# Performance work log

Hardware: AMD Instinct MI355X
Metric: run time of the kernel (lower is better)

The kernel has to match this reference:

```python
import jax, jax.numpy as jnp
import numpy as np

N_LAYERS = 3
N_HEADS = 16
EMB = 1024
HEAD_DIM = EMB // N_HEADS
BLOCK = 1024
VOCAB = 32000
LN_EPS = 1e-5


def _layernorm(x, g, b):
    mu = jnp.mean(x, axis=-1, keepdims=True)
    var = jnp.mean((x - mu) ** 2, axis=-1, keepdims=True)
    return (x - mu) * jax.lax.rsqrt(var + LN_EPS) * g + b


def setup_inputs() -> dict:
    key = jax.random.key(0)
    ks = jax.random.split(key, 20)
    s = 0.02
    inp = {
        "input_ids": jax.random.randint(ks[0], (4, 1024), 0, VOCAB),
        "targets": jax.random.randint(ks[1], (4, 1024), 0, VOCAB),
        "tok_emb": jax.random.normal(ks[2], (VOCAB, EMB), jnp.float32) * s,
        "pos_emb": jax.random.normal(ks[3], (BLOCK, EMB), jnp.float32) * s,
        # per-layer stacked params [L, ...]
        "wq": jax.random.normal(ks[4], (N_LAYERS, N_HEADS, EMB, HEAD_DIM), jnp.float32) * s,
        "wk": jax.random.normal(ks[5], (N_LAYERS, N_HEADS, EMB, HEAD_DIM), jnp.float32) * s,
        "wv": jax.random.normal(ks[6], (N_LAYERS, N_HEADS, EMB, HEAD_DIM), jnp.float32) * s,
        "wo": jax.random.normal(ks[7], (N_LAYERS, EMB, EMB), jnp.float32) * s,
        "bo": jnp.zeros((N_LAYERS, EMB), jnp.float32),
        "ln1_g": jnp.ones((N_LAYERS, EMB), jnp.float32),
        "ln1_b": jnp.zeros((N_LAYERS, EMB), jnp.float32),
        "w1": jax.random.normal(ks[8], (N_LAYERS, EMB, 4 * EMB), jnp.float32) * s,
        "b1": jnp.zeros((N_LAYERS, 4 * EMB), jnp.float32),
        "w2": jax.random.normal(ks[9], (N_LAYERS, 4 * EMB, EMB), jnp.float32) * s,
        "b2": jnp.zeros((N_LAYERS, EMB), jnp.float32),
        "lnf_g": jnp.ones((EMB,), jnp.float32),
        "lnf_b": jnp.zeros((EMB,), jnp.float32),
        "lm_w": jax.random.normal(ks[10], (EMB, VOCAB), jnp.float32) * s,
        "lm_b": jnp.zeros((VOCAB,), jnp.float32),
    }
    return inp


def _forward(input_ids, targets, tok_emb, pos_emb, wq, wk, wv, wo, bo,
             ln1_g, ln1_b, w1, b1, w2, b2, lnf_g, lnf_b, lm_w, lm_b):
    B, T = input_ids.shape
    x = tok_emb[input_ids] + pos_emb[:T]  # [B,T,E]
    scale = 1.0 / np.sqrt(EMB)  # NOTE: original scales by 1/sqrt(C)=1/sqrt(emb_dim)
    causal = jnp.tril(jnp.ones((T, T), bool))
    for l in range(N_LAYERS):
        h = _layernorm(x, ln1_g[l], ln1_b[l])
        q = jnp.einsum('bte,hed->bhtd', h, wq[l])
        k = jnp.einsum('bte,hed->bhtd', h, wk[l])
        v = jnp.einsum('bte,hed->bhtd', h, wv[l])
        wei = jnp.einsum('bhtd,bhsd->bhts', q, k) * scale
        wei = jnp.where(causal, wei, -jnp.inf)
        wei = jax.nn.softmax(wei, axis=-1)  # dropout = identity (eval)
        o = jnp.einsum('bhts,bhsd->bhtd', wei, v)
        o = o.transpose(0, 2, 1, 3).reshape(B, T, EMB)  # concat heads
        x = x + jnp.einsum('bte,ef->btf', o, wo[l]) + bo[l]
        # NOTE: original Block applies ln1 (not ln2) before the FFN too
        h2 = _layernorm(x, ln1_g[l], ln1_b[l])
        ff = jax.nn.relu(jnp.einsum('bte,ef->btf', h2, w1[l]) + b1[l])
        x = x + jnp.einsum('btf,fe->bte', ff, w2[l]) + b2[l]
    x = _layernorm(x, lnf_g, lnf_b)
    logits = jnp.einsum('bte,ev->btv', x, lm_w) + lm_b
    logits = logits.reshape(B * T, VOCAB)
    tgt = targets.reshape(B * T)
    logp = jax.nn.log_softmax(logits, axis=-1)
    loss = -jnp.mean(jnp.take_along_axis(logp, tgt[:, None], axis=-1))
    return logits, loss


def reference(input_ids, targets, tok_emb, pos_emb, wq, wk, wv, wo, bo,
              ln1_g, ln1_b, w1, b1, w2, b2, lnf_g, lnf_b, lm_w, lm_b):
    return _forward(input_ids, targets, tok_emb, pos_emb, wq, wk, wv, wo, bo,
                    ln1_g, ln1_b, w1, b1, w2, b2, lnf_g, lnf_b, lm_w, lm_b)
```

## Files before the change

### kernel.cpp

```cpp
#include <hip/hip_runtime.h>
#include <hip/hip_bf16.h>
#include <stdint.h>

#define EMB    1024
#define NH     16
#define HD     64
#define SEQ    1024
#define NBATCH 4
#define NTOK   4096
#define VOCAB  32000
#define NL     3
#define FFD    4096
#define LN_EPS 1e-5f

typedef __attribute__((ext_vector_type(8))) __bf16 bf16x8;
typedef __attribute__((ext_vector_type(4))) float  f32x4;

__device__ inline unsigned short f2b(float f) {
  __hip_bfloat16 h = __float2bfloat16(f);
  return *reinterpret_cast<unsigned short*>(&h);
}
__device__ inline float b2f(unsigned short u) {
  unsigned x = ((unsigned)u) << 16;
  return __uint_as_float(x);
}

__global__ __launch_bounds__(256) void gemm_bt(
    const unsigned short* __restrict__ A,
    const unsigned short* __restrict__ Bt,
    float* __restrict__ Cf,
    unsigned short* __restrict__ Cb,
    const float* __restrict__ resid,
    const float* __restrict__ bias,
    int M, int N, int K,
    int lda, int ldb, int ldc,
    int nb2, long sa1, long sa2, long sb1, long sb2, long sc1, long sc2,
    float scale, int flags)
{
  __shared__ __align__(16) unsigned short As[128 * 40];
  __shared__ __align__(16) unsigned short Bs[128 * 40];

  int z  = blockIdx.z;
  int i1 = z / nb2, i2 = z - i1 * nb2;
  long aoff = (long)i1 * sa1 + (long)i2 * sa2;
  long boff = (long)i1 * sb1 + (long)i2 * sb2;
  long coff = (long)i1 * sc1 + (long)i2 * sc2;

  int n0 = blockIdx.x * 128;
  int m0 = blockIdx.y * 128;

  int t    = threadIdx.x;
  int wave = t >> 6, lane = t & 63;
  int wm   = wave >> 1, wn = wave & 1;
  int quad = lane >> 4, l16 = lane & 15;

  f32x4 acc[4][4];
#pragma unroll
  for (int i = 0; i < 4; ++i)
#pragma unroll
    for (int j = 0; j < 4; ++j)
      acc[i][j] = (f32x4){0.f, 0.f, 0.f, 0.f};

  int r_st = t >> 2;
  int s_st = t & 3;

  for (int kt = 0; kt < K; kt += 32) {
    __syncthreads();
#pragma unroll
    for (int it = 0; it < 2; ++it) {
      int r  = r_st + it * 64;
      int gk = kt + s_st * 8;
      uint4 va = make_uint4(0u, 0u, 0u, 0u);
      int gm = m0 + r;
      if (gm < M) va = *(const uint4*)(A + aoff + (long)gm * lda + gk);
      *(uint4*)&As[r * 40 + s_st * 8] = va;
      uint4 vb = make_uint4(0u, 0u, 0u, 0u);
      int gn = n0 + r;
      if (gn < N) vb = *(const uint4*)(Bt + boff + (long)gn * ldb + gk);
      *(uint4*)&Bs[r * 40 + s_st * 8] = vb;
    }
    __syncthreads();

    bf16x8 af[4], bv[4];
#pragma unroll
    for (int i = 0; i < 4; ++i)
      af[i] = *(const bf16x8*)&As[(wm * 64 + i * 16 + l16) * 40 + quad * 8];
#pragma unroll
    for (int j = 0; j < 4; ++j)
      bv[j] = *(const bf16x8*)&Bs[(wn * 64 + j * 16 + l16) * 40 + quad * 8];
#pragma unroll
    for (int i = 0; i < 4; ++i)
#pragma unroll
      for (int j = 0; j < 4; ++j)
        acc[i][j] = __builtin_amdgcn_mfma_f32_16x16x32_bf16(af[i], bv[j], acc[i][j], 0, 0, 0);
  }

#pragma unroll
  for (int i = 0; i < 4; ++i) {
#pragma unroll
    for (int j = 0; j < 4; ++j) {
#pragma unroll
      for (int r = 0; r < 4; ++r) {
        int m = m0 + wm * 64 + i * 16 + quad * 4 + r;
        int n = n0 + wn * 64 + j * 16 + l16;
        if (m < M && n < N) {
          float v = acc[i][j][r] * scale;
          if ((flags & 2) && n > m) v = -__builtin_inff();
          if (bias)  v += bias[n];
          if (resid) v += resid[coff + (long)m * ldc + n];
          if (flags & 1) v = fmaxf(v, 0.f);
          long off = coff + (long)m * ldc + n;
          if (Cb) Cb[off] = f2b(v);
          else    Cf[off] = v;
        }
      }
    }
  }
}

__global__ void transpose_fb(const float* __restrict__ in, unsigned short* __restrict__ out,
                             int R, int C, int ld_in,
                             int nb2, long is1, long is2, long os1, long os2)
{
  __shared__ float tile[32][33];
  int z = blockIdx.z;
  int i1 = z / nb2, i2 = z - i1 * nb2;
  const float* ip = in + (long)i1 * is1 + (long)i2 * is2;
  unsigned short* op = out + (long)i1 * os1 + (long)i2 * os2;
  int c0 = blockIdx.x * 32, r0 = blockIdx.y * 32;
  int tx = threadIdx.x, ty = threadIdx.y;
#pragma unroll
  for (int i = 0; i < 32; i += 8) {
    int r = r0 + ty + i, c = c0 + tx;
    if (r < R && c < C) tile[ty + i][tx] = ip[(long)r * ld_in + c];
  }
  __syncthreads();
#pragma unroll
  for (int i = 0; i < 32; i += 8) {
    int c = c0 + ty + i, r = r0 + tx;
    if (r < R && c < C) op[(long)c * R + r] = f2b(tile[tx][ty + i]);
  }
}

__global__ void transpose_bb(const unsigned short* __restrict__ in, unsigned short* __restrict__ out,
                             int R, int C, int ld_in,
                             int nb2, long is1, long is2, long os1, long os2)
{
  __shared__ unsigned short tile[32][33];
  int z = blockIdx.z;
  int i1 = z / nb2, i2 = z - i1 * nb2;
  const unsigned short* ip = in + (long)i1 * is1 + (long)i2 * is2;
  unsigned short* op = out + (long)i1 * os1 + (long)i2 * os2;
  int c0 = blockIdx.x * 32, r0 = blockIdx.y * 32;
  int tx = threadIdx.x, ty = threadIdx.y;
#pragma unroll
  for (int i = 0; i < 32; i += 8) {
    int r = r0 + ty + i, c = c0 + tx;
    if (r < R && c < C) tile[ty + i][tx] = ip[(long)r * ld_in + c];
  }
  __syncthreads();
#pragma unroll
  for (int i = 0; i < 32; i += 8) {
    int c = c0 + ty + i, r = r0 + tx;
    if (r < R && c < C) op[(long)c * R + r] = tile[tx][ty + i];
  }
}

__global__ void embed_k(const int* __restrict__ ids, const float* __restrict__ tok,
                        const float* __restrict__ pos, float* __restrict__ x)
{
  int row = blockIdx.x;
  int tp  = row & (SEQ - 1);
  int id  = ids[row];
  const float* tr = tok + (long)id * EMB;
  const float* pr = pos + (long)tp * EMB;
  float* xr = x + (long)row * EMB;
  for (int i = threadIdx.x; i < EMB; i += 256) xr[i] = tr[i] + pr[i];
}

__global__ void ln_k(const float* __restrict__ x, const float* __restrict__ g,
                     const float* __restrict__ b, unsigned short* __restrict__ h)
{
  __shared__ float sm[8];
  int row = blockIdx.x;
  const float* xr = x + (long)row * EMB;
  float v[4]; float s = 0.f, s2 = 0.f;
#pragma unroll
  for (int i = 0; i < 4; ++i) {
    v[i] = xr[threadIdx.x + i * 256];
    s += v[i]; s2 += v[i] * v[i];
  }
  for (int off = 32; off > 0; off >>= 1) {
    s  += __shfl_down(s,  off, 64);
    s2 += __shfl_down(s2, off, 64);
  }
  int wave = threadIdx.x >> 6, lane = threadIdx.x & 63;
  if (lane == 0) { sm[wave * 2] = s; sm[wave * 2 + 1] = s2; }
  __syncthreads();
  s  = sm[0] + sm[2] + sm[4] + sm[6];
  s2 = sm[1] + sm[3] + sm[5] + sm[7];
  float mu  = s * (1.f / EMB);
  float var = s2 * (1.f / EMB) - mu * mu;
  float inv = rsqrtf(var + LN_EPS);
  unsigned short* hr = h + (long)row * EMB;
#pragma unroll
  for (int i = 0; i < 4; ++i) {
    int e = threadIdx.x + i * 256;
    hr[e] = f2b((v[i] - mu) * inv * g[e] + b[e]);
  }
}

__global__ void softmax_k(unsigned short* __restrict__ S)
{
  __shared__ float sm[4];
  long row = blockIdx.x;
  unsigned short* r = S + row * 1024;
  float v[4]; float mx = -__builtin_inff();
#pragma unroll
  for (int i = 0; i < 4; ++i) { v[i] = b2f(r[threadIdx.x + i * 256]); mx = fmaxf(mx, v[i]); }
  for (int off = 32; off > 0; off >>= 1) mx = fmaxf(mx, __shfl_down(mx, off, 64));
  int wave = threadIdx.x >> 6, lane = threadIdx.x & 63;
  if (lane == 0) sm[wave] = mx;
  __syncthreads();
  mx = fmaxf(fmaxf(sm[0], sm[1]), fmaxf(sm[2], sm[3]));
  __syncthreads();
  float e[4]; float s = 0.f;
#pragma unroll
  for (int i = 0; i < 4; ++i) { e[i] = __expf(v[i] - mx); s += e[i]; }
  for (int off = 32; off > 0; off >>= 1) s += __shfl_down(s, off, 64);
  if (lane == 0) sm[wave] = s;
  __syncthreads();
  s = sm[0] + sm[1] + sm[2] + sm[3];
  float inv = 1.f / s;
#pragma unroll
  for (int i = 0; i < 4; ++i) r[threadIdx.x + i * 256] = f2b(e[i] * inv);
}

__global__ void loss_rows_k(const float* __restrict__ logits, const int* __restrict__ tgt,
                            float* __restrict__ rowloss)
{
  __shared__ float smm[4], sms[4];
  int row = blockIdx.x;
  const float* lr = logits + (long)row * VOCAB;
  float m = -__builtin_inff(), s = 0.f;
  for (int i = threadIdx.x; i < VOCAB; i += 256) {
    float x = lr[i];
    float nm = fmaxf(m, x);
    s = s * __expf(m - nm) + __expf(x - nm);
    m = nm;
  }
  for (int off = 32; off > 0; off >>= 1) {
    float om = __shfl_down(m, off, 64);
    float os = __shfl_down(s, off, 64);
    float nm = fmaxf(m, om);
    s = s * __expf(m - nm) + os * __expf(om - nm);
    m = nm;
  }
  int wave = threadIdx.x >> 6, lane = threadIdx.x & 63;
  if (lane == 0) { smm[wave] = m; sms[wave] = s; }
  __syncthreads();
  if (threadIdx.x == 0) {
    float M0 = fmaxf(fmaxf(smm[0], smm[1]), fmaxf(smm[2], smm[3]));
    float S0 = 0.f;
    for (int w = 0; w < 4; ++w) S0 += sms[w] * __expf(smm[w] - M0);
    rowloss[row] = M0 + logf(S0) - lr[tgt[row]];
  }
}

__global__ void loss_reduce_k(const float* __restrict__ rowloss, float* __restrict__ out)
{
  __shared__ float sm[4];
  float s = 0.f;
  for (int i = threadIdx.x; i < NTOK; i += 256) s += rowloss[i];
  for (int off = 32; off > 0; off >>= 1) s += __shfl_down(s, off, 64);
  int wave = threadIdx.x >> 6, lane = threadIdx.x & 63;
  if (lane == 0) sm[wave] = s;
  __syncthreads();
  if (threadIdx.x == 0) out[0] = (sm[0] + sm[1] + sm[2] + sm[3]) * (1.f / NTOK);
}

extern "C" void kernel_launch(void* const* d_in, const int* in_sizes, int n_in,
                              void* d_out, int out_size, void* d_ws, size_t ws_size,
                              hipStream_t stream)
{
  const int*   ids  = (const int*)d_in[0];
  const int*   tgt  = (const int*)d_in[1];
  const float* tok  = (const float*)d_in[2];
  const float* pos  = (const float*)d_in[3];
  const float* wq   = (const float*)d_in[4];
  const float* wk   = (const float*)d_in[5];
  const float* wv   = (const float*)d_in[6];
  const float* wo   = (const float*)d_in[7];
  const float* bo   = (const float*)d_in[8];
  const float* ln1g = (const float*)d_in[9];
  const float* ln1b = (const float*)d_in[10];
  const float* w1   = (const float*)d_in[11];
  const float* b1   = (const float*)d_in[12];
  const float* w2   = (const float*)d_in[13];
  const float* b2   = (const float*)d_in[14];
  const float* lnfg = (const float*)d_in[15];
  const float* lnfb = (const float*)d_in[16];
  const float* lmw  = (const float*)d_in[17];
  const float* lmb  = (const float*)d_in[18];

  float* logits = (float*)d_out;
  float* loss   = logits + (long)NTOK * VOCAB;

  char* p = (char*)d_ws;
  auto alloc = [&](size_t bytes) { char* q = p; p += (bytes + 255) & ~(size_t)255; return q; };
  float*          x    = (float*)alloc((size_t)NTOK * EMB * 4);
  unsigned short* h    = (unsigned short*)alloc((size_t)NTOK * EMB * 2);
  unsigned short* qkv  = (unsigned short*)alloc((size_t)NTOK * 3 * EMB * 2);
  unsigned short* vT   = (unsigned short*)alloc((size_t)NBATCH * NH * HD * SEQ * 2);
  unsigned short* S    = (unsigned short*)alloc((size_t)NBATCH * NH * SEQ * SEQ * 2);
  unsigned short* o    = (unsigned short*)alloc((size_t)NTOK * EMB * 2);
  unsigned short* ff   = (unsigned short*)alloc((size_t)NTOK * FFD * 2);
  unsigned short* Wqkv = (unsigned short*)alloc((size_t)NL * 3 * EMB * EMB * 2);
  unsigned short* Wo   = (unsigned short*)alloc((size_t)NL * EMB * EMB * 2);
  unsigned short* W1   = (unsigned short*)alloc((size_t)NL * EMB * FFD * 2);
  unsigned short* W2   = (unsigned short*)alloc((size_t)NL * EMB * FFD * 2);
  unsigned short* LM   = (unsigned short*)alloc((size_t)VOCAB * EMB * 2);
  float*          rls  = (float*)alloc((size_t)NTOK * 4);

  dim3 tb(32, 8);
  const long LEE = (long)EMB * EMB;

  for (int l = 0; l < NL; ++l) {
    transpose_fb<<<dim3(2, 32, 16), tb, 0, stream>>>(wq + (long)l * NH * EMB * HD,
        Wqkv + (long)l * 3 * LEE,            EMB, HD, HD, 16, 0, (long)EMB * HD, 0, (long)HD * EMB);
    transpose_fb<<<dim3(2, 32, 16), tb, 0, stream>>>(wk + (long)l * NH * EMB * HD,
        Wqkv + (long)l * 3 * LEE + LEE,      EMB, HD, HD, 16, 0, (long)EMB * HD, 0, (long)HD * EMB);
    transpose_fb<<<dim3(2, 32, 16), tb, 0, stream>>>(wv + (long)l * NH * EMB * HD,
        Wqkv + (long)l * 3 * LEE + 2 * LEE,  EMB, HD, HD, 16, 0, (long)EMB * HD, 0, (long)HD * EMB);
    transpose_fb<<<dim3(32, 32, 1), tb, 0, stream>>>(wo + l * LEE, Wo + l * LEE,
        EMB, EMB, EMB, 1, 0, 0, 0, 0);
    transpose_fb<<<dim3(128, 32, 1), tb, 0, stream>>>(w1 + (long)l * EMB * FFD, W1 + (long)l * EMB * FFD,
        EMB, FFD, FFD, 1, 0, 0, 0, 0);
    transpose_fb<<<dim3(32, 128, 1), tb, 0, stream>>>(w2 + (long)l * EMB * FFD, W2 + (long)l * EMB * FFD,
        FFD, EMB, EMB, 1, 0, 0, 0, 0);
  }
  transpose_fb<<<dim3(1000, 32, 1), tb, 0, stream>>>(lmw, LM, EMB, VOCAB, VOCAB, 1, 0, 0, 0, 0);

  embed_k<<<NTOK, 256, 0, stream>>>(ids, tok, pos, x);

  for (int l = 0; l < NL; ++l) {
    const float* g1  = ln1g + l * EMB;
    const float* bb1 = ln1b + l * EMB;

    ln_k<<<NTOK, 256, 0, stream>>>(x, g1, bb1, h);

    gemm_bt<<<dim3(24, 32, 1), 256, 0, stream>>>(h, Wqkv + (long)l * 3 * LEE, nullptr, qkv,
        nullptr, nullptr, NTOK, 3 * EMB, EMB, EMB, EMB, 3 * EMB,
        1, 0, 0, 0, 0, 0, 0, 1.f, 0);

    transpose_bb<<<dim3(2, 32, NBATCH * NH), tb, 0, stream>>>(qkv + 2 * EMB, vT,
        SEQ, HD, 3 * EMB, NH, (long)SEQ * 3 * EMB, (long)HD, (long)NH * HD * SEQ, (long)HD * SEQ);

    gemm_bt<<<dim3(8, 8, NBATCH * NH), 256, 0, stream>>>(qkv, qkv + EMB, nullptr, S,
        nullptr, nullptr, SEQ, SEQ, HD, 3 * EMB, 3 * EMB, SEQ,
        NH, (long)SEQ * 3 * EMB, (long)HD, (long)SEQ * 3 * EMB, (long)HD,
        (long)NH * SEQ * SEQ, (long)SEQ * SEQ, 0.03125f, 2);

    softmax_k<<<NBATCH * NH * SEQ, 256, 0, stream>>>(S);

    gemm_bt<<<dim3(1, 8, NBATCH * NH), 256, 0, stream>>>(S, vT, nullptr, o,
        nullptr, nullptr, SEQ, HD, SEQ, SEQ, SEQ, EMB,
        NH, (long)NH * SEQ * SEQ, (long)SEQ * SEQ, (long)NH * HD * SEQ, (long)HD * SEQ,
        (long)SEQ * EMB, (long)HD, 1.f, 0);

    gemm_bt<<<dim3(8, 32, 1), 256, 0, stream>>>(o, Wo + l * LEE, x, nullptr,
        x, bo + l * EMB, NTOK, EMB, EMB, EMB, EMB, EMB,
        1, 0, 0, 0, 0, 0, 0, 1.f, 0);

    ln_k<<<NTOK, 256, 0, stream>>>(x, g1, bb1, h);

    gemm_bt<<<dim3(32, 32, 1), 256, 0, stream>>>(h, W1 + (long)l * EMB * FFD, nullptr, ff,
        nullptr, b1 + l * FFD, NTOK, FFD, EMB, EMB, EMB, FFD,
        1, 0, 0, 0, 0, 0, 0, 1.f, 1);

    gemm_bt<<<dim3(8, 32, 1), 256, 0, stream>>>(ff, W2 + (long)l * EMB * FFD, x, nullptr,
        x, b2 + l * EMB, NTOK, EMB, FFD, FFD, FFD, EMB,
        1, 0, 0, 0, 0, 0, 0, 1.f, 0);
  }

  ln_k<<<NTOK, 256, 0, stream>>>(x, lnfg, lnfb, h);
  gemm_bt<<<dim3(250, 32, 1), 256, 0, stream>>>(h, LM, logits, nullptr,
      nullptr, lmb, NTOK, VOCAB, EMB, EMB, EMB, VOCAB,
      1, 0, 0, 0, 0, 0, 0, 1.f, 0);

  loss_rows_k<<<NTOK, 256, 0, stream>>>(logits, tgt, rls);
  loss_reduce_k<<<1, 256, 0, stream>>>(rls, loss);
}
```

Measured before the change: 3.565 ms.

## Use direct global-to-LDS loads, XCD-aware tile remap, and skip masked causal tiles

```diff
diff --git a/kernel.cpp b/kernel.cpp
--- a/kernel.cpp
+++ b/kernel.cpp
@@ -23,6 +23,12 @@
 __device__ inline float b2f(unsigned short u) {
   unsigned x = ((unsigned)u) << 16;
   return __uint_as_float(x);
+}
+
+__device__ inline void gload16(const void* g, void* l) {
+  __builtin_amdgcn_global_load_lds(
+      (const __attribute__((address_space(1))) unsigned int*)g,
+      (__attribute__((address_space(3))) unsigned int*)l, 16, 0, 0);
 }
 
 __global__ __launch_bounds__(256) void gemm_bt(
@@ -37,8 +43,8 @@
     int nb2, long sa1, long sa2, long sb1, long sb2, long sc1, long sc2,
     float scale, int flags)
 {
-  __shared__ __align__(16) unsigned short As[128 * 40];
-  __shared__ __align__(16) unsigned short Bs[128 * 40];
+  __shared__ __align__(16) unsigned short As[128 * 32];
+  __shared__ __align__(16) unsigned short Bs[128 * 32];
 
   int z  = blockIdx.z;
   int i1 = z / nb2, i2 = z - i1 * nb2;
@@ -46,14 +52,36 @@
   long boff = (long)i1 * sb1 + (long)i2 * sb2;
   long coff = (long)i1 * sc1 + (long)i2 * sc2;
 
-  int n0 = blockIdx.x * 128;
-  int m0 = blockIdx.y * 128;
+  int flat = blockIdx.y * gridDim.x + blockIdx.x;
+  int nwg  = gridDim.x * gridDim.y;
+  if (gridDim.z == 1 && nwg > 8) {
+    int q = nwg >> 3, rq = nwg & 7;
+    int xcd = flat & 7, idx = flat >> 3;
+    flat = (xcd < rq ? xcd * (q + 1) : rq * (q + 1) + (xcd - rq) * q) + idx;
+  }
+  int n0 = (flat % gridDim.x) * 128;
+  int m0 = (flat / gridDim.x) * 128;
 
   int t    = threadIdx.x;
   int wave = t >> 6, lane = t & 63;
   int wm   = wave >> 1, wn = wave & 1;
   int quad = lane >> 4, l16 = lane & 15;
 
+  if ((flags & 2) && n0 >= m0 + 128) {
+    unsigned short ninf = f2b(-__builtin_inff());
+#pragma unroll
+    for (int i = 0; i < 4; ++i)
+#pragma unroll
+      for (int j = 0; j < 4; ++j)
+#pragma unroll
+        for (int r = 0; r < 4; ++r) {
+          int m = m0 + wm * 64 + i * 16 + quad * 4 + r;
+          int n = n0 + wn * 64 + j * 16 + l16;
+          if (m < M && n < N) Cb[coff + (long)m * ldc + n] = ninf;
+        }
+    return;
+  }
+
   f32x4 acc[4][4];
 #pragma unroll
   for (int i = 0; i < 4; ++i)
@@ -61,33 +89,29 @@
     for (int j = 0; j < 4; ++j)
       acc[i][j] = (f32x4){0.f, 0.f, 0.f, 0.f};
 
-  int r_st = t >> 2;
-  int s_st = t & 3;
+  const unsigned short* Ag = A + aoff;
+  const unsigned short* Bg = Bt + boff;
+  int srow = wave * 16 + (lane >> 2);
+  int kcol = (lane & 3) * 8;
 
   for (int kt = 0; kt < K; kt += 32) {
     __syncthreads();
 #pragma unroll
-    for (int it = 0; it < 2; ++it) {
-      int r  = r_st + it * 64;
-      int gk = kt + s_st * 8;
-      uint4 va = make_uint4(0u, 0u, 0u, 0u);
-      int gm = m0 + r;
-      if (gm < M) va = *(const uint4*)(A + aoff + (long)gm * lda + gk);
-      *(uint4*)&As[r * 40 + s_st * 8] = va;
-      uint4 vb = make_uint4(0u, 0u, 0u, 0u);
-      int gn = n0 + r;
-      if (gn < N) vb = *(const uint4*)(Bt + boff + (long)gn * ldb + gk);
-      *(uint4*)&Bs[r * 40 + s_st * 8] = vb;
+    for (int r = 0; r < 2; ++r) {
+      int gm = m0 + r * 64 + srow; if (gm >= M) gm = M - 1;
+      int gn = n0 + r * 64 + srow; if (gn >= N) gn = N - 1;
+      gload16(Ag + (long)gm * lda + kt + kcol, As + r * 2048 + wave * 512);
+      gload16(Bg + (long)gn * ldb + kt + kcol, Bs + r * 2048 + wave * 512);
     }
     __syncthreads();
 
     bf16x8 af[4], bv[4];
 #pragma unroll
     for (int i = 0; i < 4; ++i)
-      af[i] = *(const bf16x8*)&As[(wm * 64 + i * 16 + l16) * 40 + quad * 8];
+      af[i] = *(const bf16x8*)&As[(wm * 64 + i * 16 + l16) * 32 + quad * 8];
 #pragma unroll
     for (int j = 0; j < 4; ++j)
-      bv[j] = *(const bf16x8*)&Bs[(wn * 64 + j * 16 + l16) * 40 + quad * 8];
+      bv[j] = *(const bf16x8*)&Bs[(wn * 64 + j * 16 + l16) * 32 + quad * 8];
 #pragma unroll
     for (int i = 0; i < 4; ++i)
 #pragma unroll
```

New measurement: 2.973 ms. 16.6% less time.
